# Kernel optimization log

Measured on AMD Instinct MI355X. Metric: run time of the kernel, lower is better.

## Reference

```python
import jax, jax.numpy as jnp
import numpy as np

EPS = 1e-06
T1_CLIP = 1e7

B, C, M, N = 16, 3, 512, 512


def setup_inputs() -> dict:
    key = jax.random.key(0)
    k1, k2, k3, k4, k5 = jax.random.split(key, 5)
    target = jax.random.normal(k1, (B, C, M, N), dtype=jnp.float32)
    mu = jax.random.normal(k2, (B, C, M, N), dtype=jnp.float32)
    # sigma_y must be invertible per pixel: build SPD matrices A A^T + 0.5 I
    A = jax.random.normal(k3, (B, M, N, C, C), dtype=jnp.float32) * 0.3
    sigma_y = A @ jnp.swapaxes(A, -1, -2) + 0.5 * jnp.eye(C, dtype=jnp.float32)
    # sigma_mu / sigma_n are accepted by forward but unused in the loss math
    sigma_mu = jax.random.normal(k4, (B, M, N, C, C), dtype=jnp.float32)
    sigma_n = jax.random.normal(k5, (B, M, N, C, C), dtype=jnp.float32)
    return {"target": target, "mu": mu, "sigma_mu": sigma_mu,
            "sigma_n": sigma_n, "sigma_y": sigma_y}


def reference(target, mu, sigma_mu, sigma_n, sigma_y):
    # residual as per-pixel vector: [B, M, N, C]
    T = jnp.transpose(target - mu, (0, 2, 3, 1))
    inv_sy = jnp.linalg.inv(sigma_y)                      # [B,M,N,C,C]
    # quadratic form 0.5 * T^t Sigma^{-1} T per pixel -> [B,M,N]
    t1 = 0.5 * jnp.einsum('bmnc,bmncd,bmnd->bmn', T, inv_sy, T)
    dets = 0.5 * jnp.log(jnp.clip(jnp.linalg.det(sigma_y), EPS))
    loss = jnp.mean(t1 + dets)
    # torch code zeroes the loss value if t1 blows up
    loss = jnp.where(jnp.max(t1) > T1_CLIP, jnp.zeros_like(loss), loss)
    return loss
```

## Files before the change

### kernel.cpp

```cpp
#include <hip/hip_runtime.h>
#include <math.h>


#define EPS_F 1e-06f
#define T1_CLIP_F 1e7f

constexpr long long MN = 512LL * 512LL;
constexpr long long P  = 16LL * MN;
constexpr int TPB  = 256;
constexpr int PPB  = 1024;
constexpr int NBLK = (int)(P / PPB);
constexpr int SF4  = PPB * 9 / 4;

__device__ __forceinline__ void pixel_eval(
    float t0, float t1, float t2,
    float s00, float s01, float s02,
    float s10, float s11, float s12,
    float s20, float s21, float s22,
    float& t1v, float& dets)
{
    const float c00 = s11*s22 - s12*s21;
    const float c01 = s12*s20 - s10*s22;
    const float c02 = s10*s21 - s11*s20;
    const float det = s00*c00 + s01*c01 + s02*c02;

    const float a01 = s02*s21 - s01*s22;
    const float a02 = s01*s12 - s02*s11;
    const float a11 = s00*s22 - s02*s20;
    const float a12 = s02*s10 - s00*s12;
    const float a21 = s01*s20 - s00*s21;
    const float a22 = s00*s11 - s01*s10;

    const float q = t0*(c00*t0 + a01*t1 + a02*t2)
                  + t1*(c01*t0 + a11*t1 + a12*t2)
                  + t2*(c02*t0 + a21*t1 + a22*t2);

    t1v  = 0.5f * q / det;
    dets = 0.5f * logf(fmaxf(det, EPS_F));
}

__global__ __launch_bounds__(TPB) void map_partial(
    const float* __restrict__ target, const float* __restrict__ mu,
    const float* __restrict__ sigma, double* __restrict__ psum,
    float* __restrict__ pmax)
{
    __shared__ float4 sh[SF4];
    const int t = threadIdx.x;

    const long long blk_p0 = (long long)blockIdx.x * PPB;

    const float4* sp = (const float4*)sigma + blk_p0 * 9 / 4;
    #pragma unroll
    for (int k = 0; k < 9; ++k) {
        __builtin_amdgcn_global_load_lds(
            (const __attribute__((address_space(1))) void*)(sp + k * TPB + t),
            (__attribute__((address_space(3))) void*)(&sh[k * TPB + t]),
            16, 0, 0);
    }

    const long long p0 = blk_p0 + 4LL * t;
    const long long b  = p0 >> 18;
    const long long r  = p0 & (MN - 1);
    const long long tb = b * (3 * MN) + r;

    const float4 tg0 = *(const float4*)(target + tb);
    const float4 tg1 = *(const float4*)(target + tb + MN);
    const float4 tg2 = *(const float4*)(target + tb + 2*MN);
    const float4 m0  = *(const float4*)(mu + tb);
    const float4 m1  = *(const float4*)(mu + tb + MN);
    const float4 m2  = *(const float4*)(mu + tb + 2*MN);

    __syncthreads();

    const float4* f = sh + 9 * t;
    const float4 f0 = f[0], f1 = f[1], f2 = f[2];
    const float4 f3 = f[3], f4_ = f[4], f5 = f[5];
    const float4 f6 = f[6], f7 = f[7], f8 = f[8];

    double acc = 0.0;
    float mx = 0.0f;
    {
        float t1v, dets;
        pixel_eval(tg0.x - m0.x, tg1.x - m1.x, tg2.x - m2.x,
                   f0.x, f0.y, f0.z, f0.w, f1.x, f1.y, f1.z, f1.w, f2.x,
                   t1v, dets);
        acc += (double)(t1v + dets); mx = fmaxf(mx, t1v);
        pixel_eval(tg0.y - m0.y, tg1.y - m1.y, tg2.y - m2.y,
                   f2.y, f2.z, f2.w, f3.x, f3.y, f3.z, f3.w, f4_.x, f4_.y,
                   t1v, dets);
        acc += (double)(t1v + dets); mx = fmaxf(mx, t1v);
        pixel_eval(tg0.z - m0.z, tg1.z - m1.z, tg2.z - m2.z,
                   f4_.z, f4_.w, f5.x, f5.y, f5.z, f5.w, f6.x, f6.y, f6.z,
                   t1v, dets);
        acc += (double)(t1v + dets); mx = fmaxf(mx, t1v);
        pixel_eval(tg0.w - m0.w, tg1.w - m1.w, tg2.w - m2.w,
                   f6.w, f7.x, f7.y, f7.z, f7.w, f8.x, f8.y, f8.z, f8.w,
                   t1v, dets);
        acc += (double)(t1v + dets); mx = fmaxf(mx, t1v);
    }

    for (int off = 32; off > 0; off >>= 1) {
        acc += __shfl_down(acc, off, 64);
        mx = fmaxf(mx, __shfl_down(mx, off, 64));
    }
    __shared__ double ssum[TPB / 64];
    __shared__ float  smax[TPB / 64];
    const int lane = t & 63;
    const int wv   = t >> 6;
    if (lane == 0) { ssum[wv] = acc; smax[wv] = mx; }
    __syncthreads();
    if (t == 0) {
        double a = ssum[0] + ssum[1] + ssum[2] + ssum[3];
        float  m = fmaxf(fmaxf(smax[0], smax[1]), fmaxf(smax[2], smax[3]));
        psum[blockIdx.x] = a;
        pmax[blockIdx.x] = m;
    }
}

__global__ __launch_bounds__(TPB) void map_final(
    const double* __restrict__ psum, const float* __restrict__ pmax,
    float* __restrict__ out)
{
    double acc = 0.0;
    float mx = 0.0f;
    for (int i = threadIdx.x; i < NBLK; i += TPB) {
        acc += psum[i];
        mx = fmaxf(mx, pmax[i]);
    }
    for (int off = 32; off > 0; off >>= 1) {
        acc += __shfl_down(acc, off, 64);
        mx = fmaxf(mx, __shfl_down(mx, off, 64));
    }
    __shared__ double ssum[TPB / 64];
    __shared__ float  smax[TPB / 64];
    const int lane = threadIdx.x & 63;
    const int wv   = threadIdx.x >> 6;
    if (lane == 0) { ssum[wv] = acc; smax[wv] = mx; }
    __syncthreads();
    if (threadIdx.x == 0) {
        double a = ssum[0] + ssum[1] + ssum[2] + ssum[3];
        float  m = fmaxf(fmaxf(smax[0], smax[1]), fmaxf(smax[2], smax[3]));
        float loss = (float)(a / (double)P);
        out[0] = (m > T1_CLIP_F) ? 0.0f : loss;
    }
}

extern "C" void kernel_launch(void* const* d_in, const int* in_sizes, int n_in,
                              void* d_out, int out_size, void* d_ws, size_t ws_size,
                              hipStream_t stream) {
    const float* target  = (const float*)d_in[0];
    const float* mu      = (const float*)d_in[1];
    const float* sigma_y = (const float*)d_in[4];

    double* psum = (double*)d_ws;
    float*  pmax = (float*)((char*)d_ws + NBLK * sizeof(double));

    map_partial<<<NBLK, TPB, 0, stream>>>(target, mu, sigma_y, psum, pmax);
    map_final<<<1, TPB, 0, stream>>>(psum, pmax, (float*)d_out);
}
```

Before: 392.4 us.

## Software-pipeline per-wave chunks with double-buffered LDS sigma staging

```diff
diff --git a/kernel.cpp b/kernel.cpp
--- a/kernel.cpp
+++ b/kernel.cpp
@@ -7,10 +7,13 @@
 
 constexpr long long MN = 512LL * 512LL;
 constexpr long long P  = 16LL * MN;
-constexpr int TPB  = 256;
-constexpr int PPB  = 1024;
-constexpr int NBLK = (int)(P / PPB);
-constexpr int SF4  = PPB * 9 / 4;
+constexpr int TPB   = 256;
+constexpr int WAVES = TPB / 64;
+constexpr int CHPX  = 256;
+constexpr int CHF4  = CHPX * 9 / 4;
+constexpr int CPW   = 8;
+constexpr long long NCHUNK = P / CHPX;
+constexpr int NBLK  = (int)(NCHUNK / (CPW * WAVES));
 
 __device__ __forceinline__ void pixel_eval(
     float t0, float t1, float t2,
@@ -39,74 +42,91 @@
     dets = 0.5f * logf(fmaxf(det, EPS_F));
 }
 
-__global__ __launch_bounds__(TPB) void map_partial(
+__global__ __launch_bounds__(TPB, 2) void map_partial(
     const float* __restrict__ target, const float* __restrict__ mu,
     const float* __restrict__ sigma, double* __restrict__ psum,
     float* __restrict__ pmax)
 {
-    __shared__ float4 sh[SF4];
-    const int t = threadIdx.x;
+    __shared__ float4 sh[WAVES][2][CHF4];
+    const int t    = threadIdx.x;
+    const int lane = t & 63;
+    const int wv   = t >> 6;
 
-    const long long blk_p0 = (long long)blockIdx.x * PPB;
-
-    const float4* sp = (const float4*)sigma + blk_p0 * 9 / 4;
-    #pragma unroll
-    for (int k = 0; k < 9; ++k) {
-        __builtin_amdgcn_global_load_lds(
-            (const __attribute__((address_space(1))) void*)(sp + k * TPB + t),
-            (__attribute__((address_space(3))) void*)(&sh[k * TPB + t]),
-            16, 0, 0);
-    }
-
-    const long long p0 = blk_p0 + 4LL * t;
-    const long long b  = p0 >> 18;
-    const long long r  = p0 & (MN - 1);
-    const long long tb = b * (3 * MN) + r;
-
-    const float4 tg0 = *(const float4*)(target + tb);
-    const float4 tg1 = *(const float4*)(target + tb + MN);
-    const float4 tg2 = *(const float4*)(target + tb + 2*MN);
-    const float4 m0  = *(const float4*)(mu + tb);
-    const float4 m1  = *(const float4*)(mu + tb + MN);
-    const float4 m2  = *(const float4*)(mu + tb + 2*MN);
-
-    __syncthreads();
-
-    const float4* f = sh + 9 * t;
-    const float4 f0 = f[0], f1 = f[1], f2 = f[2];
-    const float4 f3 = f[3], f4_ = f[4], f5 = f[5];
-    const float4 f6 = f[6], f7 = f[7], f8 = f[8];
+    const long long gw  = (long long)blockIdx.x * WAVES + wv;
+    const long long ck0 = gw * CPW;
 
     double acc = 0.0;
-    float mx = 0.0f;
-    {
+    float  mx  = 0.0f;
+    float4 TG[2][3], MM[2][3];
+
+    auto stage = [&](int par, long long ck) {
+        const float4* sp = (const float4*)sigma + ck * CHF4;
+        #pragma unroll
+        for (int k = 0; k < 9; ++k) {
+            __builtin_amdgcn_global_load_lds(
+                (const __attribute__((address_space(1))) void*)(sp + k * 64 + lane),
+                (__attribute__((address_space(3))) void*)(&sh[wv][par][k * 64 + lane]),
+                16, 0, 0);
+        }
+    };
+    auto loadTM = [&](long long ck, float4* T4, float4* M4) {
+        const long long p0 = ck * CHPX + 4LL * lane;
+        const long long b  = p0 >> 18;
+        const long long r  = p0 & (MN - 1);
+        const long long tb = b * (3 * MN) + r;
+        T4[0] = *(const float4*)(target + tb);
+        T4[1] = *(const float4*)(target + tb + MN);
+        T4[2] = *(const float4*)(target + tb + 2 * MN);
+        M4[0] = *(const float4*)(mu + tb);
+        M4[1] = *(const float4*)(mu + tb + MN);
+        M4[2] = *(const float4*)(mu + tb + 2 * MN);
+    };
+    auto compute = [&](int par, const float4* T4, const float4* M4) {
+        const float4* f = &sh[wv][par][0] + 9 * lane;
+        const float4 f0 = f[0], f1 = f[1], f2 = f[2];
+        const float4 f3 = f[3], f4_ = f[4], f5 = f[5];
+        const float4 f6 = f[6], f7 = f[7], f8 = f[8];
         float t1v, dets;
-        pixel_eval(tg0.x - m0.x, tg1.x - m1.x, tg2.x - m2.x,
+        pixel_eval(T4[0].x - M4[0].x, T4[1].x - M4[1].x, T4[2].x - M4[2].x,
                    f0.x, f0.y, f0.z, f0.w, f1.x, f1.y, f1.z, f1.w, f2.x,
                    t1v, dets);
         acc += (double)(t1v + dets); mx = fmaxf(mx, t1v);
-        pixel_eval(tg0.y - m0.y, tg1.y - m1.y, tg2.y - m2.y,
+        pixel_eval(T4[0].y - M4[0].y, T4[1].y - M4[1].y, T4[2].y - M4[2].y,
                    f2.y, f2.z, f2.w, f3.x, f3.y, f3.z, f3.w, f4_.x, f4_.y,
                    t1v, dets);
         acc += (double)(t1v + dets); mx = fmaxf(mx, t1v);
-        pixel_eval(tg0.z - m0.z, tg1.z - m1.z, tg2.z - m2.z,
+        pixel_eval(T4[0].z - M4[0].z, T4[1].z - M4[1].z, T4[2].z - M4[2].z,
                    f4_.z, f4_.w, f5.x, f5.y, f5.z, f5.w, f6.x, f6.y, f6.z,
                    t1v, dets);
         acc += (double)(t1v + dets); mx = fmaxf(mx, t1v);
-        pixel_eval(tg0.w - m0.w, tg1.w - m1.w, tg2.w - m2.w,
+        pixel_eval(T4[0].w - M4[0].w, T4[1].w - M4[1].w, T4[2].w - M4[2].w,
                    f6.w, f7.x, f7.y, f7.z, f7.w, f8.x, f8.y, f8.z, f8.w,
                    t1v, dets);
         acc += (double)(t1v + dets); mx = fmaxf(mx, t1v);
+    };
+
+    stage(0, ck0);
+    loadTM(ck0, TG[0], MM[0]);
+
+    #pragma unroll
+    for (int cc = 0; cc < CPW; ++cc) {
+        if (cc + 1 < CPW) {
+            asm volatile("s_waitcnt lgkmcnt(0)" ::: "memory");
+            stage((cc + 1) & 1, ck0 + cc + 1);
+            loadTM(ck0 + cc + 1, TG[(cc + 1) & 1], MM[(cc + 1) & 1]);
+            asm volatile("s_waitcnt vmcnt(15)" ::: "memory");
+        } else {
+            asm volatile("s_waitcnt vmcnt(0)" ::: "memory");
+        }
+        compute(cc & 1, TG[cc & 1], MM[cc & 1]);
     }
 
     for (int off = 32; off > 0; off >>= 1) {
         acc += __shfl_down(acc, off, 64);
         mx = fmaxf(mx, __shfl_down(mx, off, 64));
     }
-    __shared__ double ssum[TPB / 64];
-    __shared__ float  smax[TPB / 64];
-    const int lane = t & 63;
-    const int wv   = t >> 6;
+    __shared__ double ssum[WAVES];
+    __shared__ float  smax[WAVES];
     if (lane == 0) { ssum[wv] = acc; smax[wv] = mx; }
     __syncthreads();
     if (t == 0) {
```

New measurement: 395.3 us. About the same (+0.7%).
